# Optimization experiments

Measured on AMD Instinct MI355X. Metric: run time of the kernel, lower is better.

## Reference

```python
import jax, jax.numpy as jnp
import numpy as np

B, S, D = 1, 2048, 1024
H, HD = 16, 64          # attention heads, head dim
DFF = 4096              # ffn hidden
IH, ID = 4, 64          # indexer heads / dim ('baseline' strategy)
TOP_K = 64
ROPE_BASE = 10000.0
LN_EPS = 1e-5


def setup_inputs() -> dict:
    key = jax.random.key(0)
    ks = jax.random.split(key, 12)
    g = lambda k, shape: (jax.random.normal(k, shape, dtype=jnp.float32) * 0.02)
    return {
        "x": jax.random.normal(ks[0], (B, S, D), dtype=jnp.float32),
        "w_qkv": g(ks[1], (D, 3 * D)),
        "w_o": g(ks[2], (D, D)),
        "ffn_w1": g(ks[3], (D, DFF)),
        "ffn_b1": jnp.zeros((DFF,), jnp.float32),
        "ffn_w2": g(ks[4], (DFF, D)),
        "ffn_b2": jnp.zeros((D,), jnp.float32),
        "ln1_g": jnp.ones((D,), jnp.float32),
        "ln1_b": jnp.zeros((D,), jnp.float32),
        "ln2_g": jnp.ones((D,), jnp.float32),
        "ln2_b": jnp.zeros((D,), jnp.float32),
        "idx_wq": g(ks[5], (D, IH * ID)),
        "idx_wk": g(ks[6], (D, ID)),
        "idx_ww": g(ks[7], (D, IH)),
    }


def _layernorm(x, g, b):
    m = jnp.mean(x, axis=-1, keepdims=True)
    v = jnp.var(x, axis=-1, keepdims=True)
    return (x - m) * jax.lax.rsqrt(v + LN_EPS) * g + b


def _rope(x):  # x: [B,S,H,HD], torchtune interleaved-pair convention
    half = HD // 2
    theta = 1.0 / (ROPE_BASE ** (jnp.arange(0, HD, 2, dtype=jnp.float32) / HD))  # [half]
    ang = jnp.arange(S, dtype=jnp.float32)[:, None] * theta                      # [S,half]
    cos = jnp.cos(ang)[None, :, None, :]
    sin = jnp.sin(ang)[None, :, None, :]
    xp = x.reshape(*x.shape[:-1], half, 2)
    x0, x1 = xp[..., 0], xp[..., 1]
    out = jnp.stack([x0 * cos - x1 * sin, x1 * cos + x0 * sin], axis=-1)
    return out.reshape(x.shape)


def reference(x, w_qkv, w_o, ffn_w1, ffn_b1, ffn_w2, ffn_b2,
              ln1_g, ln1_b, ln2_g, ln2_b, idx_wq, idx_wk, idx_ww):
    norm_x = _layernorm(x, ln1_g, ln1_b)

    qkv = norm_x @ w_qkv                              # [B,S,3D]
    q, k, v = jnp.split(qkv, 3, axis=-1)
    q = _rope(q.reshape(B, S, H, HD))
    k = _rope(k.reshape(B, S, H, HD))
    v = v.reshape(B, S, H, HD)

    # Lightning-style indexer: I[t,s] = sum_h w[t,h] * relu(q_i[t,h] . k_i[s])
    qi = (norm_x @ idx_wq).reshape(B, S, IH, ID)      # [B,S,IH,ID]
    ki = norm_x @ idx_wk                              # [B,S,ID]
    wi = norm_x @ idx_ww                              # [B,S,IH]
    qk = jnp.einsum("bthd,bsd->bths", qi, ki)         # [B,S,IH,S]
    index_scores = jnp.einsum("bth,bths->bts", wi, jax.nn.relu(qk))  # [B,S,S]

    # causal top-k token selection -> boolean mask
    causal = jnp.tril(jnp.ones((S, S), dtype=bool))
    masked_scores = jnp.where(causal, index_scores, -jnp.inf)
    _, topk_idx = jax.lax.top_k(masked_scores, TOP_K)  # [B,S,K]
    b_ix = jnp.arange(B)[:, None, None]
    q_ix = jnp.arange(S)[None, :, None]
    mask = jnp.zeros((B, S, S), dtype=bool).at[b_ix, q_ix, topk_idx].set(True)
    mask = mask & causal                               # [B,S,S]

    # masked SDPA
    logits = jnp.einsum("bqhd,bkhd->bhqk", q, k) / np.sqrt(HD)
    logits = jnp.where(mask[:, None, :, :], logits, -jnp.inf)
    attn = jax.nn.softmax(logits, axis=-1)
    attn_out = jnp.einsum("bhqk,bkhd->bqhd", attn, v).reshape(B, S, D)
    x = x + attn_out @ w_o

    h = _layernorm(x, ln2_g, ln2_b)
    ffn = jax.nn.gelu(h @ ffn_w1 + ffn_b1, approximate=False) @ ffn_w2 + ffn_b2
    return x + ffn
```

## Files before the change

kernel.cpp:

```cpp
#include <hip/hip_runtime.h>
#include <math.h>

#define S_LEN 2048
#define D_MODEL 1024
#define NHEAD 16
#define HDIM 64
#define DFF 4096
#define IH 4
#define IDM 64
#define TOPK 64
#define NIDX 336

typedef float f32x4 __attribute__((ext_vector_type(4)));
typedef short bf16x8 __attribute__((ext_vector_type(8)));

__device__ __forceinline__ unsigned short f2bf(float f) {
    unsigned u = __builtin_bit_cast(unsigned, f);
    u += 0x7fff + ((u >> 16) & 1);
    return (unsigned short)(u >> 16);
}
__device__ __forceinline__ float bf2f(unsigned short us) {
    return __builtin_bit_cast(float, (unsigned)us << 16);
}

__device__ __forceinline__ float gelu_exact(float v) {
    return 0.5f * v * (1.f + erff(v * 0.70710678118654752f));
}

__device__ __forceinline__ void gl_lds16(const void* g, void* l) {
    __builtin_amdgcn_global_load_lds(
        (const __attribute__((address_space(1))) void*)g,
        (__attribute__((address_space(3))) void*)l, 16, 0, 0);
}

__global__ __launch_bounds__(256) void ln_kernel(const float* __restrict__ x,
    const float* __restrict__ g, const float* __restrict__ b,
    float* __restrict__ outf, unsigned short* __restrict__ outb)
{
    int row = blockIdx.x, tid = threadIdx.x;
    const float4 v = *(const float4*)(x + (size_t)row * D_MODEL + tid * 4);
    float s = v.x + v.y + v.z + v.w;
    float ss = v.x * v.x + v.y * v.y + v.z * v.z + v.w * v.w;
    int lane = tid & 63, wv = tid >> 6;
    for (int o = 32; o; o >>= 1) { s += __shfl_xor(s, o); ss += __shfl_xor(ss, o); }
    __shared__ float rs[4], rss[4];
    if (lane == 0) { rs[wv] = s; rss[wv] = ss; }
    __syncthreads();
    float S = rs[0] + rs[1] + rs[2] + rs[3];
    float SS = rss[0] + rss[1] + rss[2] + rss[3];
    float mean = S * (1.f / D_MODEL);
    float var = SS * (1.f / D_MODEL) - mean * mean;
    float r = rsqrtf(var + 1e-5f);
    float4 gv = *(const float4*)(g + tid * 4);
    float4 bv = *(const float4*)(b + tid * 4);
    float4 o4;
    o4.x = (v.x - mean) * r * gv.x + bv.x;
    o4.y = (v.y - mean) * r * gv.y + bv.y;
    o4.z = (v.z - mean) * r * gv.z + bv.z;
    o4.w = (v.w - mean) * r * gv.w + bv.w;
    if (outf) *(float4*)(outf + (size_t)row * D_MODEL + tid * 4) = o4;
    if (outb) {
        ushort4 u4 = { f2bf(o4.x), f2bf(o4.y), f2bf(o4.z), f2bf(o4.w) };
        *(ushort4*)(outb + (size_t)row * D_MODEL + tid * 4) = u4;
    }
}

__global__ __launch_bounds__(256) void wtrans_kernel(const float* __restrict__ in,
    unsigned short* __restrict__ out, int K, int N)
{
    __shared__ float t[32][33];
    int k0 = blockIdx.y * 32, n0 = blockIdx.x * 32;
    int tid = threadIdx.x;
    int r = tid >> 5, c = tid & 31;
#pragma unroll
    for (int p = 0; p < 4; ++p)
        t[r + p * 8][c] = in[(size_t)(k0 + r + p * 8) * N + n0 + c];
    __syncthreads();
#pragma unroll
    for (int p = 0; p < 4; ++p)
        out[(size_t)(n0 + r + p * 8) * K + k0 + c] = f2bf(t[c][r + p * 8]);
}

__global__ __launch_bounds__(256) void wpack_kernel(const float* __restrict__ wq,
    const float* __restrict__ wk, const float* __restrict__ ww, float* __restrict__ Wc)
{
    int idx = blockIdx.x * 256 + threadIdx.x;
    if (idx >= D_MODEL * NIDX) return;
    int r = idx / NIDX, c = idx % NIDX;
    float v = 0.f;
    if (c < 256) v = wq[r * 256 + c];
    else if (c < 320) v = wk[r * 64 + (c - 256)];
    else if (c < 324) v = ww[r * 4 + (c - 320)];
    Wc[idx] = v;
}

__global__ __launch_bounds__(256) void gemm_bf16_n64(
    const unsigned short* __restrict__ A, const unsigned short* __restrict__ Bt,
    float* __restrict__ C, unsigned short* __restrict__ Cb,
    const float* __restrict__ bias, const float* __restrict__ R,
    int M, int N, int K, int act,
    float* __restrict__ P, int kchunk)
{
    __shared__ __attribute__((aligned(16))) unsigned short As[128 * 32];
    __shared__ __attribute__((aligned(16))) unsigned short Bs[64 * 32];
    int tid = threadIdx.x;
    int bm = blockIdx.y * 128, bn = blockIdx.x * 64;
    int wid = tid >> 6, lane = tid & 63;
    int wm = wid * 32;
    const unsigned short* Ab = A + (size_t)bm * K;
    const unsigned short* Bb = Bt + (size_t)bn * K;
    f32x4 acc[2][4];
#pragma unroll
    for (int i = 0; i < 2; ++i)
#pragma unroll
        for (int j = 0; j < 4; ++j)
            acc[i][j] = (f32x4){0.f, 0.f, 0.f, 0.f};

    int kbeg = blockIdx.z * kchunk;
    int kend = kbeg + kchunk;
    int fr = lane & 15, fk = (lane >> 4) * 8;
    int e0 = tid * 8;
    int r0 = e0 >> 5, c0 = e0 & 31;
    for (int k0 = kbeg; k0 < kend; k0 += 32) {
        gl_lds16(Ab + (size_t)r0 * K + k0 + c0, As + e0);
        gl_lds16(Ab + (size_t)(r0 + 64) * K + k0 + c0, As + e0 + 2048);
        gl_lds16(Bb + (size_t)r0 * K + k0 + c0, Bs + e0);
        __syncthreads();
        bf16x8 af[2], bfv[4];
#pragma unroll
        for (int mi = 0; mi < 2; ++mi)
            af[mi] = *(const bf16x8*)&As[(wm + mi * 16 + fr) * 32 + fk];
#pragma unroll
        for (int ni = 0; ni < 4; ++ni)
            bfv[ni] = *(const bf16x8*)&Bs[(ni * 16 + fr) * 32 + fk];
#pragma unroll
        for (int mi = 0; mi < 2; ++mi)
#pragma unroll
            for (int ni = 0; ni < 4; ++ni)
                acc[mi][ni] = __builtin_amdgcn_mfma_f32_16x16x32_bf16(
                    af[mi], bfv[ni], acc[mi][ni], 0, 0, 0);
        __syncthreads();
    }
    int cl = lane & 15, rh = (lane >> 4) * 4;
    if (P) {
        float* Pz = P + (size_t)blockIdx.z * M * N;
#pragma unroll
        for (int mi = 0; mi < 2; ++mi)
#pragma unroll
            for (int ni = 0; ni < 4; ++ni) {
                int col = bn + ni * 16 + cl;
#pragma unroll
                for (int r = 0; r < 4; ++r) {
                    int row = bm + wm + mi * 16 + rh + r;
                    Pz[(size_t)row * N + col] = acc[mi][ni][r];
                }
            }
        return;
    }
#pragma unroll
    for (int mi = 0; mi < 2; ++mi) {
#pragma unroll
        for (int ni = 0; ni < 4; ++ni) {
            int col = bn + ni * 16 + cl;
            float bv = bias ? bias[col] : 0.f;
#pragma unroll
            for (int r = 0; r < 4; ++r) {
                int row = bm + wm + mi * 16 + rh + r;
                float v = acc[mi][ni][r] + bv;
                if (act) v = gelu_exact(v);
                size_t off = (size_t)row * N + col;
                if (R) v += R[off];
                if (C) C[off] = v;
                if (Cb) Cb[off] = f2bf(v);
            }
        }
    }
}

__global__ __launch_bounds__(256) void kreduce_kernel(const float* __restrict__ P,
    int nslice, float* __restrict__ C, const float* __restrict__ bias,
    const float* __restrict__ R, int M, int N)
{
    size_t total4 = (size_t)M * N / 4;
    size_t stride = (size_t)gridDim.x * 256;
    for (size_t i4 = blockIdx.x * 256 + threadIdx.x; i4 < total4; i4 += stride) {
        size_t off = i4 * 4;
        float4 v = *(const float4*)(P + off);
        for (int z = 1; z < nslice; ++z) {
            float4 p = *(const float4*)(P + (size_t)z * M * N + off);
            v.x += p.x; v.y += p.y; v.z += p.z; v.w += p.w;
        }
        if (bias) {
            float4 b4 = *(const float4*)(bias + (off % N));
            v.x += b4.x; v.y += b4.y; v.z += b4.z; v.w += b4.w;
        }
        if (R) {
            float4 r4 = *(const float4*)(R + off);
            v.x += r4.x; v.y += r4.y; v.z += r4.z; v.w += r4.w;
        }
        *(float4*)(C + off) = v;
    }
}

__global__ __launch_bounds__(256) void gemm64(const float* __restrict__ A,
    const float* __restrict__ B, float* __restrict__ C,
    int M, int N, int K,
    float* __restrict__ P, int kchunk)
{
    __shared__ float As[16][68];
    __shared__ float Bs[16][68];
    int tid = threadIdx.x;
    int bm = blockIdx.y, bn = blockIdx.x;
    int tx = tid & 15, ty = tid >> 4;
    int arow = tid >> 2;
    int acol = (tid & 3) << 2;
    int brow = tid >> 4;
    int bcol = (tid & 15) << 2;
    const float* Abase = A + (size_t)(bm * 64 + arow) * K + acol;
    float c[4][4] = {};
    int kbeg = blockIdx.z * kchunk;
    int kend = kbeg + kchunk;
    for (int k0 = kbeg; k0 < kend; k0 += 16) {
        float4 av = *(const float4*)(Abase + k0);
        As[acol + 0][arow] = av.x;
        As[acol + 1][arow] = av.y;
        As[acol + 2][arow] = av.z;
        As[acol + 3][arow] = av.w;
        int gcol = bn * 64 + bcol;
        const float* Bb = B + (size_t)(k0 + brow) * N;
        float4 bv;
        if (gcol + 3 < N) {
            bv = *(const float4*)(Bb + gcol);
        } else {
            bv.x = (gcol + 0 < N) ? Bb[gcol + 0] : 0.f;
            bv.y = (gcol + 1 < N) ? Bb[gcol + 1] : 0.f;
            bv.z = (gcol + 2 < N) ? Bb[gcol + 2] : 0.f;
            bv.w = (gcol + 3 < N) ? Bb[gcol + 3] : 0.f;
        }
        *(float4*)&Bs[brow][bcol] = bv;
        __syncthreads();
#pragma unroll
        for (int kk = 0; kk < 16; ++kk) {
            float4 a4 = *(const float4*)&As[kk][ty * 4];
            float4 b4 = *(const float4*)&Bs[kk][tx * 4];
            float av4[4] = { a4.x, a4.y, a4.z, a4.w };
            float bv4[4] = { b4.x, b4.y, b4.z, b4.w };
#pragma unroll
            for (int i = 0; i < 4; ++i)
#pragma unroll
                for (int j = 0; j < 4; ++j)
                    c[i][j] += av4[i] * bv4[j];
        }
        __syncthreads();
    }
    float* Out = P ? (P + (size_t)blockIdx.z * M * N) : C;
#pragma unroll
    for (int i = 0; i < 4; ++i) {
        int row = bm * 64 + ty * 4 + i;
#pragma unroll
        for (int j = 0; j < 4; ++j) {
            int col = bn * 64 + tx * 4 + j;
            if (col < N)
                Out[(size_t)row * N + col] = c[i][j];
        }
    }
}

__global__ __launch_bounds__(256) void rope_table_kernel(float* __restrict__ ct, float* __restrict__ st)
{
    int g = blockIdx.x * 256 + threadIdx.x;
    int t = g >> 5, i = g & 31;
    float theta = powf(10000.f, -(float)i / 32.f);
    float ang = (float)t * theta;
    ct[g] = cosf(ang);
    st[g] = sinf(ang);
}

__global__ __launch_bounds__(512) void rope_pack_kernel(
    const unsigned short* __restrict__ qkvb,
    const float* __restrict__ ct, const float* __restrict__ st,
    unsigned short* __restrict__ Qb, unsigned short* __restrict__ Kb,
    unsigned short* __restrict__ Vb)
{
    int t = blockIdx.x, tid = threadIdx.x;
    int h = tid >> 5, i = tid & 31;
    float c = ct[t * 32 + i], s = st[t * 32 + i];
    const unsigned short* base = qkvb + (size_t)t * (3 * D_MODEL);
    ushort2 q2 = *(const ushort2*)(base + h * HDIM + 2 * i);
    float q0 = bf2f(q2.x), q1 = bf2f(q2.y);
    ushort2 qo = { f2bf(q0 * c - q1 * s), f2bf(q1 * c + q0 * s) };
    *(ushort2*)(Qb + (size_t)t * D_MODEL + h * HDIM + 2 * i) = qo;
    ushort2 k2 = *(const ushort2*)(base + D_MODEL + h * HDIM + 2 * i);
    float k0 = bf2f(k2.x), k1 = bf2f(k2.y);
    ushort2 ko = { f2bf(k0 * c - k1 * s), f2bf(k1 * c + k0 * s) };
    *(ushort2*)(Kb + ((size_t)h * S_LEN + t) * HDIM + 2 * i) = ko;
    ushort2 v2 = *(const ushort2*)(base + 2 * D_MODEL + 2 * tid);
    int vh = tid >> 5, vd = (2 * tid) & 63;
    *(ushort2*)(Vb + ((size_t)vh * S_LEN + t) * HDIM + vd) = v2;
}

__global__ __launch_bounds__(256) void scores_kernel(const float* __restrict__ QIW,
    float* __restrict__ scores)
{
    int t0 = blockIdx.y * 32, s0 = blockIdx.x * 32;
    if (s0 > t0 + 31) return;
    __shared__ float qis[32][256];
    __shared__ float kis[32][65];
    __shared__ float wis[32][4];
    int tid = threadIdx.x;
#pragma unroll
    for (int l = 0; l < 8; ++l) {
        int idx = l * 256 + tid;
        int r = idx >> 6, c = (idx & 63) << 2;
        *(float4*)&qis[r][c] = *(const float4*)(QIW + (size_t)(t0 + r) * NIDX + c);
    }
#pragma unroll
    for (int l = 0; l < 8; ++l) {
        int idx = l * 256 + tid;
        int r = idx >> 6, c = idx & 63;
        kis[r][c] = QIW[(size_t)(s0 + r) * NIDX + 256 + c];
    }
    if (tid < 32) *(float4*)&wis[tid][0] = *(const float4*)(QIW + (size_t)(t0 + tid) * NIDX + 320);
    __syncthreads();
    int sl = tid & 31;
    int tb = (tid >> 5) * 4;
    float acc[4] = { 0.f, 0.f, 0.f, 0.f };
#pragma unroll
    for (int h = 0; h < 4; ++h) {
        float dots[4] = { 0.f, 0.f, 0.f, 0.f };
        for (int d = 0; d < 64; ++d) {
            float kv = kis[sl][d];
#pragma unroll
            for (int i = 0; i < 4; ++i)
                dots[i] += qis[tb + i][h * 64 + d] * kv;
        }
#pragma unroll
        for (int i = 0; i < 4; ++i)
            acc[i] += wis[tb + i][h] * fmaxf(dots[i], 0.f);
    }
#pragma unroll
    for (int i = 0; i < 4; ++i)
        scores[(size_t)(t0 + tb + i) * S_LEN + s0 + sl] = acc[i];
}

__global__ __launch_bounds__(256) void topk_kernel(const float* __restrict__ scores,
    int* __restrict__ topidx, int* __restrict__ topcnt)
{
    int t = blockIdx.x, tid = threadIdx.x;
    int n = t + 1;
    if (n <= TOPK) {
        if (tid < n) topidx[t * TOPK + tid] = tid;
        if (tid == 0) topcnt[t] = n;
        return;
    }
    __shared__ unsigned sc[S_LEN];
    __shared__ unsigned hist[256];
    __shared__ int selbin_s;
    __shared__ int cnt_out;
    __shared__ unsigned wsum[4];
    for (int j = tid; j < n; j += 256) {
        unsigned u = __builtin_bit_cast(unsigned, scores[(size_t)t * S_LEN + j]);
        sc[j] = (u & 0x80000000u) ? ~u : (u | 0x80000000u);
    }
    if (tid == 0) cnt_out = 0;
    int lane = tid & 63, wv = tid >> 6;
    unsigned prefix = 0;
    int kk = TOPK;
#pragma unroll
    for (int round = 0; round < 4; ++round) {
        int shift_pref = 32 - 8 * round;
        int shift_bin = 24 - 8 * round;
        hist[tid] = 0;
        __syncthreads();
        for (int j = tid; j < n; j += 256) {
            unsigned v = sc[j];
            if ((((unsigned long long)(v ^ prefix)) >> shift_pref) == 0)
                atomicAdd(&hist[(v >> shift_bin) & 0xff], 1u);
        }
        __syncthreads();
        if (wv == 0) {
            unsigned h0 = hist[4 * lane], h1 = hist[4 * lane + 1];
            unsigned h2 = hist[4 * lane + 2], h3 = hist[4 * lane + 3];
            unsigned s3 = h3, s2 = h2 + s3, s1 = h1 + s2, s0 = h0 + s1;
            unsigned acc = s0;
            for (int off = 1; off < 64; off <<= 1) {
                unsigned o = __shfl_down(acc, off);
                if (lane + off < 64) acc += o;
            }
            unsigned above = acc - s0;
            hist[4 * lane]     = s0 + above;
            hist[4 * lane + 1] = s1 + above;
            hist[4 * lane + 2] = s2 + above;
            hist[4 * lane + 3] = s3 + above;
        }
        __syncthreads();
        {
            unsigned sufb = hist[tid];
            unsigned sufn = (tid < 255) ? hist[tid + 1] : 0u;
            if (sufb >= (unsigned)kk && sufn < (unsigned)kk)
                selbin_s = tid;
        }
        __syncthreads();
        int b = selbin_s;
        unsigned above = (b < 255) ? hist[b + 1] : 0u;
        kk -= (int)above;
        prefix |= ((unsigned)b) << shift_bin;
        __syncthreads();
    }
    unsigned T = prefix;
    int chunk = (n + 255) >> 8;
    int jb = tid * chunk;
    int je = jb + chunk; if (je > n) je = n;
    int ties = 0;
    for (int j = jb; j < je; ++j) {
        unsigned v = sc[j];
        if (v > T) { int o = atomicAdd(&cnt_out, 1); topidx[t * TOPK + o] = j; }
        else if (v == T) ++ties;
    }
    unsigned inc = (unsigned)ties;
    for (int off = 1; off < 64; off <<= 1) {
        unsigned o = __shfl_up(inc, off);
        if (lane >= off) inc += o;
    }
    if (lane == 63) wsum[wv] = inc;
    __syncthreads();
    unsigned woff = 0;
    for (int w = 0; w < wv; ++w) woff += wsum[w];
    int rank = (int)(woff + inc) - ties;
    for (int j = jb; j < je && rank < kk; ++j) {
        if (sc[j] == T) {
            int o = atomicAdd(&cnt_out, 1);
            topidx[t * TOPK + o] = j;
            ++rank;
        }
    }
    if (tid == 0) topcnt[t] = TOPK;
}

__global__ __launch_bounds__(256) void attn_kernel(
    const unsigned short* __restrict__ Qb, const unsigned short* __restrict__ Kb,
    const unsigned short* __restrict__ Vb,
    const int* __restrict__ topidx, const int* __restrict__ topcnt,
    unsigned short* __restrict__ out)
{
    int t = blockIdx.x, tid = threadIdx.x;
    __shared__ int sel[TOPK];
    if (tid < TOPK) sel[tid] = topidx[t * TOPK + tid];
    __syncthreads();
    int cnt = topcnt[t];
    int lane = tid & 63, wv = tid >> 6;
    int h = blockIdx.y * 4 + wv;
    int klo = lane >> 3, oct = lane & 7;
    int rows[8];
    bool valid[8];
#pragma unroll
    for (int kg = 0; kg < 8; ++kg) {
        int k = kg * 8 + klo;
        valid[kg] = (k < cnt);
        rows[kg] = sel[valid[kg] ? k : 0];
    }
    bf16x8 q8 = *(const bf16x8*)(Qb + (size_t)t * D_MODEL + h * HDIM + oct * 8);
    float qf[8];
#pragma unroll
    for (int e = 0; e < 8; ++e) qf[e] = bf2f((unsigned short)q8[e]);

    const unsigned short* kbase = Kb + (size_t)h * S_LEN * HDIM + oct * 8;
    float p[8];
#pragma unroll
    for (int kg = 0; kg < 8; ++kg) {
        bf16x8 k8 = *(const bf16x8*)(kbase + (size_t)rows[kg] * HDIM);
        float d = 0.f;
#pragma unroll
        for (int e = 0; e < 8; ++e)
            d += bf2f((unsigned short)k8[e]) * qf[e];
        d += __shfl_xor(d, 1);
        d += __shfl_xor(d, 2);
        d += __shfl_xor(d, 4);
        p[kg] = valid[kg] ? d * 0.125f : -INFINITY;
    }
    float m = p[0];
#pragma unroll
    for (int kg = 1; kg < 8; ++kg) m = fmaxf(m, p[kg]);
    m = fmaxf(m, __shfl_xor(m, 8));
    m = fmaxf(m, __shfl_xor(m, 16));
    m = fmaxf(m, __shfl_xor(m, 32));
    float sum = 0.f;
#pragma unroll
    for (int kg = 0; kg < 8; ++kg) { p[kg] = __expf(p[kg] - m); sum += p[kg]; }
    sum += __shfl_xor(sum, 8);
    sum += __shfl_xor(sum, 16);
    sum += __shfl_xor(sum, 32);
    float rs = 1.f / sum;
    const unsigned short* vbase = Vb + (size_t)h * S_LEN * HDIM + oct * 8;
    float facc[8] = {};
#pragma unroll
    for (int kg = 0; kg < 8; ++kg) {
        bf16x8 v8 = *(const bf16x8*)(vbase + (size_t)rows[kg] * HDIM);
        float pw = p[kg] * rs;
#pragma unroll
        for (int e = 0; e < 8; ++e)
            facc[e] += pw * bf2f((unsigned short)v8[e]);
    }
#pragma unroll
    for (int e = 0; e < 8; ++e) {
        facc[e] += __shfl_xor(facc[e], 8);
        facc[e] += __shfl_xor(facc[e], 16);
        facc[e] += __shfl_xor(facc[e], 32);
    }
    if (klo == 0) {
        ushort4 o0 = { f2bf(facc[0]), f2bf(facc[1]), f2bf(facc[2]), f2bf(facc[3]) };
        ushort4 o1 = { f2bf(facc[4]), f2bf(facc[5]), f2bf(facc[6]), f2bf(facc[7]) };
        *(ushort4*)(out + (size_t)t * D_MODEL + h * HDIM + oct * 8) = o0;
        *(ushort4*)(out + (size_t)t * D_MODEL + h * HDIM + oct * 8 + 4) = o1;
    }
}

extern "C" void kernel_launch(void* const* d_in, const int* in_sizes, int n_in,
                              void* d_out, int out_size, void* d_ws, size_t ws_size,
                              hipStream_t stream)
{
    const float* x      = (const float*)d_in[0];
    const float* w_qkv  = (const float*)d_in[1];
    const float* w_o    = (const float*)d_in[2];
    const float* ffn_w1 = (const float*)d_in[3];
    const float* ffn_b1 = (const float*)d_in[4];
    const float* ffn_w2 = (const float*)d_in[5];
    const float* ffn_b2 = (const float*)d_in[6];
    const float* ln1_g  = (const float*)d_in[7];
    const float* ln1_b  = (const float*)d_in[8];
    const float* ln2_g  = (const float*)d_in[9];
    const float* ln2_b  = (const float*)d_in[10];
    const float* idx_wq = (const float*)d_in[11];
    const float* idx_wk = (const float*)d_in[12];
    const float* idx_ww = (const float*)d_in[13];
    float* outp = (float*)d_out;

    const size_t MB = 1ull << 20;
    char* ws = (char*)d_ws;
    float*          normx    = (float*)(ws + 0);
    unsigned short* attno_bf = (unsigned short*)(ws + 0);
    float*          Pf2      = (float*)(ws + 0);
    unsigned short* normx_bf = (unsigned short*)(ws + 8 * MB);
    unsigned short* h2_bf    = normx_bf;
    unsigned short* qkv_bf   = (unsigned short*)(ws + 12 * MB);
    int*            topidx   = (int*)(ws + 12 * MB);
    int*            topcnt   = (int*)(ws + 12 * MB + 512 * 1024);
    unsigned short* wqkv_t   = (unsigned short*)(ws + 24 * MB);
    unsigned short* wo_t     = (unsigned short*)(ws + 30 * MB);
    unsigned short* w1_t     = (unsigned short*)(ws + 32 * MB);
    unsigned short* w2_t     = (unsigned short*)(ws + 40 * MB);
    unsigned short* Qb       = (unsigned short*)(ws + 48 * MB);
    unsigned short* Kb       = (unsigned short*)(ws + 52 * MB);
    unsigned short* Vb       = (unsigned short*)(ws + 56 * MB);
    float*          ctab     = (float*)(ws + 60 * MB);
    float*          stab     = (float*)(ws + 60 * MB + 256 * 1024);
    float*          P_idx    = (float*)(ws + 60 * MB);
    float*          scoresb  = (float*)(ws + 60 * MB);
    float*          Pwo      = (float*)(ws + 60 * MB);
    unsigned short* ffn1_bf  = (unsigned short*)(ws + 60 * MB);
    float*          QIW      = (float*)(ws + 76 * MB);
    float*          Wc       = (float*)(ws + 79 * MB);

    dim3 blk256(256);
    auto g64n = [](int N, int M) { return dim3(N / 64, M / 128); };

    ln_kernel<<<S_LEN, blk256, 0, stream>>>(x, ln1_g, ln1_b, normx, normx_bf);
    rope_table_kernel<<<(S_LEN * 32) / 256, blk256, 0, stream>>>(ctab, stab);
    wtrans_kernel<<<dim3(3 * D_MODEL / 32, D_MODEL / 32), blk256, 0, stream>>>(w_qkv, wqkv_t, D_MODEL, 3 * D_MODEL);
    wtrans_kernel<<<dim3(D_MODEL / 32, D_MODEL / 32), blk256, 0, stream>>>(w_o, wo_t, D_MODEL, D_MODEL);
    wtrans_kernel<<<dim3(DFF / 32, D_MODEL / 32), blk256, 0, stream>>>(ffn_w1, w1_t, D_MODEL, DFF);
    wtrans_kernel<<<dim3(D_MODEL / 32, DFF / 32), blk256, 0, stream>>>(ffn_w2, w2_t, DFF, D_MODEL);
    wpack_kernel<<<(D_MODEL * NIDX + 255) / 256, blk256, 0, stream>>>(idx_wq, idx_wk, idx_ww, Wc);
    gemm_bf16_n64<<<g64n(3 * D_MODEL, S_LEN), blk256, 0, stream>>>(normx_bf, wqkv_t,
        nullptr, qkv_bf, nullptr, nullptr, S_LEN, 3 * D_MODEL, D_MODEL, 0, nullptr, D_MODEL);
    rope_pack_kernel<<<S_LEN, dim3(512), 0, stream>>>(qkv_bf, ctab, stab, Qb, Kb, Vb);
    gemm64<<<dim3((NIDX + 63) / 64, S_LEN / 64, 4), blk256, 0, stream>>>(normx, Wc,
        nullptr, S_LEN, NIDX, D_MODEL, P_idx, D_MODEL / 4);
    kreduce_kernel<<<1024, blk256, 0, stream>>>(P_idx, 4, QIW, nullptr, nullptr, S_LEN, NIDX);
    scores_kernel<<<dim3(64, 64), blk256, 0, stream>>>(QIW, scoresb);
    topk_kernel<<<S_LEN, blk256, 0, stream>>>(scoresb, topidx, topcnt);
    attn_kernel<<<dim3(S_LEN, 4), blk256, 0, stream>>>(Qb, Kb, Vb, topidx, topcnt, attno_bf);
    gemm_bf16_n64<<<dim3(D_MODEL / 64, S_LEN / 128, 2), blk256, 0, stream>>>(attno_bf, wo_t,
        nullptr, nullptr, nullptr, nullptr, S_LEN, D_MODEL, D_MODEL, 0, Pwo, D_MODEL / 2);
    kreduce_kernel<<<1024, blk256, 0, stream>>>(Pwo, 2, outp, nullptr, x, S_LEN, D_MODEL);
    ln_kernel<<<S_LEN, blk256, 0, stream>>>(outp, ln2_g, ln2_b, nullptr, h2_bf);
    gemm_bf16_n64<<<g64n(DFF, S_LEN), blk256, 0, stream>>>(h2_bf, w1_t,
        nullptr, ffn1_bf, ffn_b1, nullptr, S_LEN, DFF, D_MODEL, 1, nullptr, D_MODEL);
    gemm_bf16_n64<<<dim3(D_MODEL / 64, S_LEN / 128, 4), blk256, 0, stream>>>(ffn1_bf, w2_t,
        nullptr, nullptr, nullptr, nullptr, S_LEN, D_MODEL, DFF, 0, Pf2, DFF / 4);
    kreduce_kernel<<<1024, blk256, 0, stream>>>(Pf2, 4, outp, ffn_b2, outp, S_LEN, D_MODEL);
}
```

Baseline: 280.6 us.

## Double-buffer LDS tiles and XOR-swizzle layout in bf16 GEMM

The GEMM main loop now uses two LDS buffers, so the next K-slice is loaded from global memory while MFMAs run on the current one. This removes the load-then-sync stall at the top of each iteration. The LDS layout is also XOR-swizzled on 8-element chunks, applied consistently on the store and fragment-read sides, to reduce bank conflicts. The cost is twice the shared memory per block, which may lower occupancy. Correctness depends on how gl_lds16 completion is ordered relative to the single barrier left in each iteration.

```diff
diff --git a/kernel.cpp b/kernel.cpp
--- a/kernel.cpp
+++ b/kernel.cpp
@@ -101,8 +101,8 @@
     int M, int N, int K, int act,
     float* __restrict__ P, int kchunk)
 {
-    __shared__ __attribute__((aligned(16))) unsigned short As[128 * 32];
-    __shared__ __attribute__((aligned(16))) unsigned short Bs[64 * 32];
+    __shared__ __attribute__((aligned(16))) unsigned short As[2][128 * 32];
+    __shared__ __attribute__((aligned(16))) unsigned short Bs[2][64 * 32];
     int tid = threadIdx.x;
     int bm = blockIdx.y * 128, bn = blockIdx.x * 64;
     int wid = tid >> 6, lane = tid & 63;
@@ -118,21 +118,32 @@
 
     int kbeg = blockIdx.z * kchunk;
     int kend = kbeg + kchunk;
-    int fr = lane & 15, fk = (lane >> 4) * 8;
-    int e0 = tid * 8;
-    int r0 = e0 >> 5, c0 = e0 & 31;
+    int fr = lane & 15;
+    int srow = tid >> 2;
+    int cels = (((tid & 3) ^ (srow & 3)) << 3);
+    int dste = tid * 8;
+    int selm = (((lane >> 4) ^ (fr & 3)) << 3);
+
+    gl_lds16(Ab + (size_t)srow * K + kbeg + cels, &As[0][dste]);
+    gl_lds16(Ab + (size_t)(srow + 64) * K + kbeg + cels, &As[0][dste + 2048]);
+    gl_lds16(Bb + (size_t)srow * K + kbeg + cels, &Bs[0][dste]);
+    __syncthreads();
+
+    int cur = 0;
     for (int k0 = kbeg; k0 < kend; k0 += 32) {
-        gl_lds16(Ab + (size_t)r0 * K + k0 + c0, As + e0);
-        gl_lds16(Ab + (size_t)(r0 + 64) * K + k0 + c0, As + e0 + 2048);
-        gl_lds16(Bb + (size_t)r0 * K + k0 + c0, Bs + e0);
-        __syncthreads();
+        int nxt = k0 + 32;
+        if (nxt < kend) {
+            gl_lds16(Ab + (size_t)srow * K + nxt + cels, &As[cur ^ 1][dste]);
+            gl_lds16(Ab + (size_t)(srow + 64) * K + nxt + cels, &As[cur ^ 1][dste + 2048]);
+            gl_lds16(Bb + (size_t)srow * K + nxt + cels, &Bs[cur ^ 1][dste]);
+        }
         bf16x8 af[2], bfv[4];
 #pragma unroll
         for (int mi = 0; mi < 2; ++mi)
-            af[mi] = *(const bf16x8*)&As[(wm + mi * 16 + fr) * 32 + fk];
+            af[mi] = *(const bf16x8*)&As[cur][(wm + mi * 16 + fr) * 32 + selm];
 #pragma unroll
         for (int ni = 0; ni < 4; ++ni)
-            bfv[ni] = *(const bf16x8*)&Bs[(ni * 16 + fr) * 32 + fk];
+            bfv[ni] = *(const bf16x8*)&Bs[cur][(ni * 16 + fr) * 32 + selm];
 #pragma unroll
         for (int mi = 0; mi < 2; ++mi)
 #pragma unroll
@@ -140,6 +151,7 @@
                 acc[mi][ni] = __builtin_amdgcn_mfma_f32_16x16x32_bf16(
                     af[mi], bfv[ni], acc[mi][ni], 0, 0, 0);
         __syncthreads();
+        cur ^= 1;
     }
     int cl = lane & 15, rh = (lane >> 4) * 4;
     if (P) {
```

New measurement: 276.4 us. Within noise of the previous version (-1.5%).
